# Performance work log

Hardware: AMD Instinct MI355X
Metric: run time of the kernel (lower is better)

The kernel has to match this reference:

```python
import jax, jax.numpy as jnp
import numpy as np

N = 4096
FEAT = 5
H = 128
L = 3
K = 4
HD = H // K  # 32


def setup_inputs() -> dict:
    key = jax.random.key(0)
    ks = jax.random.split(key, 24)
    node_features = jax.random.normal(ks[0], (N, FEAT), dtype=jnp.float32)
    u = jax.random.uniform(ks[1], (N, N), dtype=jnp.float32)
    adj = jnp.where(u < 0.01, u, 0.0)
    adj = adj / (adj.sum(axis=1, keepdims=True) + 1e-8)  # row-normalised
    mask = jax.random.randint(ks[2], (N,), 0, 2).astype(bool)
    s = 0.05
    return {
        'node_features': node_features,
        'adj': adj,
        'mask': mask,
        'Wi': jax.random.normal(ks[3], (FEAT, H), jnp.float32) * s,
        'bi': jnp.zeros((H,), jnp.float32),
        'gat_W': jax.random.normal(ks[4], (L, K, H, HD), jnp.float32) * s,
        'gat_a': jax.random.normal(ks[5], (L, K, 2 * HD), jnp.float32) * s,
        'ln_g': jnp.ones((L, H), jnp.float32),
        'ln_b': jnp.zeros((L, H), jnp.float32),
        'pW1': jax.random.normal(ks[6], (H, H // 2), jnp.float32) * s,
        'pb1': jnp.zeros((H // 2,), jnp.float32),
        'pW2': jax.random.normal(ks[7], (H // 2, 1), jnp.float32) * s,
        'pb2': jnp.zeros((1,), jnp.float32),
        'poolW': jax.random.normal(ks[8], (H, H), jnp.float32) * s,
        'poolb': jnp.zeros((H,), jnp.float32),
        'poolv': jax.random.normal(ks[9], (H,), jnp.float32) * s,
        'vW1': jax.random.normal(ks[10], (H, H // 2), jnp.float32) * s,
        'vb1': jnp.zeros((H // 2,), jnp.float32),
        'vW2': jax.random.normal(ks[11], (H // 2, 1), jnp.float32) * s,
        'vb2': jnp.zeros((1,), jnp.float32),
    }


def _layernorm(x, g, b, eps=1e-5):
    mu = x.mean(-1, keepdims=True)
    var = ((x - mu) ** 2).mean(-1, keepdims=True)
    return (x - mu) / jnp.sqrt(var + eps) * g + b


def reference(node_features, adj, mask, Wi, bi, gat_W, gat_a, ln_g, ln_b,
              pW1, pb1, pW2, pb2, poolW, poolb, poolv, vW1, vb1, vW2, vb2):
    n = node_features.shape[0]
    x = jax.nn.relu(node_features @ Wi + bi)  # (N, H)
    edge_mask = (adj > 0) | jnp.eye(n, dtype=bool)  # (N, N) incl self-loops
    n_layers = gat_W.shape[0]
    for l in range(n_layers):
        Wx = jnp.einsum('nd,kdh->knh', x, gat_W[l])  # (K, N, hd)
        a_src = jnp.einsum('knh,kh->kn', Wx, gat_a[l][:, :HD])  # (K, N)
        a_dst = jnp.einsum('knh,kh->kn', Wx, gat_a[l][:, HD:])  # (K, N)
        e = jax.nn.leaky_relu(a_src[:, :, None] + a_dst[:, None, :], 0.2)  # (K,N,N)
        e = jnp.where(edge_mask[None], e, -jnp.inf)
        alpha = jax.nn.softmax(e, axis=-1)  # softmax over neighbours j
        h = jax.nn.elu(jnp.einsum('kij,kjh->kih', alpha, Wx))  # (K, N, hd)
        out = jnp.transpose(h, (1, 0, 2)).reshape(n, -1)  # concat heads -> (N, H)
        out = out + x  # residual (Identity: in_dim == out_dim)
        x = _layernorm(out, ln_g[l], ln_b[l])
    # policy head
    logits = (jax.nn.relu(x @ pW1 + pb1) @ pW2 + pb2).squeeze(-1)  # (N,)
    logits = jnp.where(mask, logits, -jnp.inf)
    # attention pooling restricted to masked (valid) nodes
    scores = jnp.tanh(x @ poolW + poolb) @ poolv  # (N,)
    scores = jnp.where(mask, scores, -jnp.inf)
    beta = jax.nn.softmax(scores)
    pooled = (beta[:, None] * x).sum(0)  # (H,)
    value = (jax.nn.relu(pooled @ vW1 + vb1) @ vW2 + vb2).squeeze(-1)  # scalar
    return logits, value
```

## Files before the change

kernel.cpp:

```cpp
#include <hip/hip_runtime.h>

#define NN 4096
#define FEAT 5
#define H 128
#define HD 32
#define KH 4
#define NEG_INF (-__builtin_inff())
#define MASK_SENTINEL (-1e30f)

#define WS_FLAG  0
#define WS_DEG   256
#define WS_NBR   (WS_DEG + NN*4)
#define WS_X     (WS_NBR + NN*128*2)
#define WS_WX    (WS_X + NN*H*4)
#define WS_ATS   (WS_WX + NN*H*4)
#define WS_ATD   (WS_ATS + NN*16)
#define WS_PART  (WS_ATD + NN*16)
#define WS_ZPART (WS_PART + 256*H*4)

__device__ __forceinline__ float red64(float v) {
#pragma unroll
    for (int off = 32; off; off >>= 1) v += __shfl_xor(v, off, 64);
    return v;
}
__device__ __forceinline__ float red64max(float v) {
#pragma unroll
    for (int off = 32; off; off >>= 1) v = fmaxf(v, __shfl_xor(v, off, 64));
    return v;
}
__device__ __forceinline__ float red32(float v) {
#pragma unroll
    for (int off = 16; off; off >>= 1) v += __shfl_xor(v, off, 32);
    return v;
}
__device__ __forceinline__ bool read_mask(const void* mp, int f, int n) {
    if (f == 3) return ((const long long*)mp)[n] != 0;
    if (f == 1) return ((const int*)mp)[n] != 0;
    if (f == 2) return ((const float*)mp)[n] != 0.f;
    return ((const unsigned char*)mp)[n] != 0;
}

__global__ __launch_bounds__(256) void k_csr_proj(
    const float* __restrict__ adj, const float* __restrict__ nf,
    const float* __restrict__ Wi, const float* __restrict__ bi,
    const void* mask, int* flag, int* __restrict__ deg,
    unsigned short* __restrict__ nbr, float* __restrict__ xbuf) {
    __shared__ int ln[4][128];
    int w = threadIdx.x >> 6, lane = threadIdx.x & 63;
    int row = blockIdx.x * 4 + w;
    ln[w][lane] = 0; ln[w][64 + lane] = 0;
    const float4* arow = (const float4*)(adj + (size_t)row * NN);
    int cnt = 0;
    bool self = false;
    for (int c0 = 0; c0 < NN / 4; c0 += 64) {
        float4 v = arow[c0 + lane];
        int cb = (c0 + lane) * 4;
        float vals[4] = {v.x, v.y, v.z, v.w};
#pragma unroll
        for (int s = 0; s < 4; s++) {
            bool nz = vals[s] > 0.f;
            if (nz && cb + s == row) self = true;
            unsigned long long b = __ballot((int)nz);
            if (nz) {
                int pos = cnt + __popcll(b & ((1ull << lane) - 1ull));
                if (pos < 128) ln[w][pos] = cb + s;
            }
            cnt += __popcll(b);
        }
    }
    bool anyself = __any((int)self);
    if (!anyself) {
        if (lane == 0 && cnt < 128) ln[w][cnt] = row;
        cnt++;
    }
    int d = cnt < 128 ? cnt : 128;
    if (lane == 0) deg[row] = d;
    nbr[(size_t)row * 128 + lane] = (unsigned short)ln[w][lane];
    nbr[(size_t)row * 128 + 64 + lane] = (unsigned short)ln[w][64 + lane];
    float a1 = bi[lane], a2 = bi[64 + lane];
#pragma unroll
    for (int f = 0; f < FEAT; f++) {
        float xv = nf[row * FEAT + f];
        a1 += xv * Wi[f * H + lane];
        a2 += xv * Wi[f * H + 64 + lane];
    }
    xbuf[(size_t)row * H + lane] = fmaxf(a1, 0.f);
    xbuf[(size_t)row * H + 64 + lane] = fmaxf(a2, 0.f);
    if (blockIdx.x == 0 && w == 0) {
        const unsigned* ip = (const unsigned*)mask;
        const float* fp = (const float*)mask;
        bool i32ok = true, i64ok = true, f32ok = true;
        for (int i = lane; i < 1024; i += 64) {
            unsigned v = ip[i];
            if (v > 1u) i32ok = false;
            if (i & 1) { if (v != 0u) i64ok = false; }
            else       { if (v > 1u) i64ok = false; }
            float fv = fp[i];
            if (fv != 0.f && fv != 1.f) f32ok = false;
        }
        i32ok = (__ballot((int)i32ok) == ~0ull);
        i64ok = (__ballot((int)i64ok) == ~0ull);
        f32ok = (__ballot((int)f32ok) == ~0ull);
        if (lane == 0) *flag = i64ok ? 3 : (i32ok ? 1 : (f32ok ? 2 : 0));
    }
}

__global__ __launch_bounds__(256) void k_wx(
    const float* __restrict__ xbuf, const float* __restrict__ gw,
    const float* __restrict__ ga, float* __restrict__ Wx,
    float* __restrict__ attS, float* __restrict__ attD) {
    __shared__ float xs[8][H];
    int t = threadIdx.x;
    int k = t >> 6, lane = t & 63, dh = lane >> 5, h = lane & 31;
    int n0 = blockIdx.x * 8;
    ((float4*)xs)[t] = ((const float4*)(xbuf + (size_t)n0 * H))[t];
    __syncthreads();
    float acc[8] = {0, 0, 0, 0, 0, 0, 0, 0};
    const float* g = gw + (size_t)k * (H * HD) + h;
    for (int dd = 0; dd < 64; dd += 4) {
        int d = dh * 64 + dd;
        float w0 = g[(size_t)(d + 0) * HD];
        float w1 = g[(size_t)(d + 1) * HD];
        float w2 = g[(size_t)(d + 2) * HD];
        float w3 = g[(size_t)(d + 3) * HD];
#pragma unroll
        for (int nn = 0; nn < 8; nn++) {
            float4 xv = *(const float4*)&xs[nn][d];
            acc[nn] += xv.x * w0 + xv.y * w1 + xv.z * w2 + xv.w * w3;
        }
    }
    float aws = ga[k * 64 + h], awd = ga[k * 64 + 32 + h];
#pragma unroll
    for (int nn = 0; nn < 8; nn++) {
        float full = acc[nn] + __shfl_xor(acc[nn], 32, 64);
        float s = red32(full * aws);
        float dv = red32(full * awd);
        int n = n0 + nn;
        if (dh == 0) Wx[(size_t)n * H + k * 32 + h] = full;
        if (lane == 0) { attS[n * 4 + k] = s; attD[n * 4 + k] = dv; }
    }
}

__global__ __launch_bounds__(256) void k_agg(
    const int* __restrict__ degG, const unsigned short* __restrict__ nbrG,
    const float* __restrict__ Wxn, const float4* __restrict__ attS4,
    const float4* __restrict__ attD4, const float* __restrict__ lng,
    const float* __restrict__ lnb, float* __restrict__ xbuf) {
    __shared__ int s_nbr[4][128];
    __shared__ float s_al[4][128][4];
    int t = threadIdx.x, w = t >> 6, lane = t & 63;
    int node = blockIdx.x * 4 + w;
    int d = degG[node];
    const unsigned short* np = nbrG + (size_t)node * 128;
    int sn0 = np[lane], sn1 = np[64 + lane];
    s_nbr[w][lane] = sn0;
    s_nbr[w][64 + lane] = sn1;
    float4 aS = attS4[node];
    float4 d0 = attD4[sn0], d1 = attD4[sn1];
    bool v0 = lane < d, v1 = 64 + lane < d;
#define LRELU(x) ((x) > 0.f ? (x) : 0.2f * (x))
    float e0x = v0 ? LRELU(aS.x + d0.x) : NEG_INF;
    float e0y = v0 ? LRELU(aS.y + d0.y) : NEG_INF;
    float e0z = v0 ? LRELU(aS.z + d0.z) : NEG_INF;
    float e0w = v0 ? LRELU(aS.w + d0.w) : NEG_INF;
    float e1x = v1 ? LRELU(aS.x + d1.x) : NEG_INF;
    float e1y = v1 ? LRELU(aS.y + d1.y) : NEG_INF;
    float e1z = v1 ? LRELU(aS.z + d1.z) : NEG_INF;
    float e1w = v1 ? LRELU(aS.w + d1.w) : NEG_INF;
#undef LRELU
    float mx = red64max(fmaxf(e0x, e1x));
    float my = red64max(fmaxf(e0y, e1y));
    float mz = red64max(fmaxf(e0z, e1z));
    float mw = red64max(fmaxf(e0w, e1w));
    float p0x = v0 ? __expf(e0x - mx) : 0.f, p1x = v1 ? __expf(e1x - mx) : 0.f;
    float p0y = v0 ? __expf(e0y - my) : 0.f, p1y = v1 ? __expf(e1y - my) : 0.f;
    float p0z = v0 ? __expf(e0z - mz) : 0.f, p1z = v1 ? __expf(e1z - mz) : 0.f;
    float p0w = v0 ? __expf(e0w - mw) : 0.f, p1w = v1 ? __expf(e1w - mw) : 0.f;
    float ix = 1.f / red64(p0x + p1x);
    float iy = 1.f / red64(p0y + p1y);
    float iz = 1.f / red64(p0z + p1z);
    float iw = 1.f / red64(p0w + p1w);
    float4 a0 = make_float4(p0x * ix, p0y * iy, p0z * iz, p0w * iw);
    float4 a1 = make_float4(p1x * ix, p1y * iy, p1z * iz, p1w * iw);
    *(float4*)&s_al[w][lane][0] = a0;
    *(float4*)&s_al[w][64 + lane][0] = a1;
    int ksel = lane >> 4;
    int dim0 = 2 * lane;
    float acc0 = 0.f, acc1 = 0.f;
    int dpad = (d + 7) & ~7;
    for (int c0 = 0; c0 < dpad; c0 += 8) {
#pragma unroll
        for (int j = 0; j < 8; j++) {
            int c = c0 + j;
            int sc = s_nbr[w][c];
            float al = s_al[w][c][ksel];
            float2 v = *(const float2*)(Wxn + (size_t)sc * H + dim0);
            acc0 += al * v.x;
            acc1 += al * v.y;
        }
    }
    float2 xr = *(const float2*)(xbuf + (size_t)node * H + dim0);
    float h0 = acc0 > 0.f ? acc0 : __expf(acc0) - 1.f;
    float h1 = acc1 > 0.f ? acc1 : __expf(acc1) - 1.f;
    float o0 = h0 + xr.x, o1 = h1 + xr.y;
    float mu = red64(o0 + o1) * (1.f / H);
    float dv0 = o0 - mu, dv1 = o1 - mu;
    float var = red64(dv0 * dv0 + dv1 * dv1) * (1.f / H);
    float rstd = rsqrtf(var + 1e-5f);
    float2 ov;
    ov.x = dv0 * rstd * lng[dim0] + lnb[dim0];
    ov.y = dv1 * rstd * lng[dim0 + 1] + lnb[dim0 + 1];
    *(float2*)(xbuf + (size_t)node * H + dim0) = ov;
}

__global__ __launch_bounds__(256) void k_heads(
    const float* __restrict__ xbuf, const float* __restrict__ pW1,
    const float* __restrict__ pb1, const float* __restrict__ pW2,
    const float* __restrict__ pb2, const float* __restrict__ poolW,
    const float* __restrict__ poolb, const float* __restrict__ poolv,
    const void* mask, const int* __restrict__ flag, float* __restrict__ out,
    float* __restrict__ part, float* __restrict__ zpart) {
    __shared__ float lds_x[16][H];
    __shared__ float lds_part[4][H];
    __shared__ float lds_z[4];
    int t = threadIdx.x, w = t >> 6, lane = t & 63;
    int n0b = blockIdx.x * 16;
    for (int idx = t; idx < 16 * H; idx += 256)
        lds_x[idx >> 7][idx & 127] = xbuf[(size_t)(n0b + (idx >> 7)) * H + (idx & 127)];
    __syncthreads();
    int nb = n0b + w * 4;
    float accp[4] = {0, 0, 0, 0}, acs1[4] = {0, 0, 0, 0}, acs2[4] = {0, 0, 0, 0};
#pragma unroll 2
    for (int d = 0; d < H; d++) {
        float w1 = pW1[d * 64 + lane];
        float q1 = poolW[d * H + lane];
        float q2 = poolW[d * H + 64 + lane];
#pragma unroll
        for (int nn = 0; nn < 4; nn++) {
            float xv = lds_x[w * 4 + nn][d];
            accp[nn] += xv * w1;
            acs1[nn] += xv * q1;
            acs2[nn] += xv * q2;
        }
    }
    int flg = *flag;
    float T = fminf(red64(fabsf(poolv[lane]) + fabsf(poolv[64 + lane])), 30.f);
    float pb1v = pb1[lane], pw2v = pW2[lane], pb2v = pb2[0];
    float pob1 = poolb[lane], pob2 = poolb[64 + lane];
    float pov1 = poolv[lane], pov2 = poolv[64 + lane];
    float pp1 = 0.f, pp2 = 0.f, zacc = 0.f;
#pragma unroll
    for (int nn = 0; nn < 4; nn++) {
        int node = nb + nn;
        float hp = red64(fmaxf(accp[nn] + pb1v, 0.f) * pw2v);
        float sc = red64(tanhf(acs1[nn] + pob1) * pov1 + tanhf(acs2[nn] + pob2) * pov2);
        bool mk = read_mask(mask, flg, node);
        if (lane == 0) out[node] = mk ? (hp + pb2v) : MASK_SENTINEL;
        float wn = mk ? __expf(sc - T) : 0.f;
        pp1 += wn * lds_x[w * 4 + nn][lane];
        pp2 += wn * lds_x[w * 4 + nn][64 + lane];
        zacc += wn;
    }
    lds_part[w][lane] = pp1;
    lds_part[w][64 + lane] = pp2;
    if (lane == 0) lds_z[w] = zacc;
    __syncthreads();
    if (w == 0) {
        float s1 = lds_part[0][lane] + lds_part[1][lane] + lds_part[2][lane] + lds_part[3][lane];
        float s2 = lds_part[0][64 + lane] + lds_part[1][64 + lane] +
                   lds_part[2][64 + lane] + lds_part[3][64 + lane];
        part[blockIdx.x * H + lane] = s1;
        part[blockIdx.x * H + 64 + lane] = s2;
        if (lane == 0) zpart[blockIdx.x] = lds_z[0] + lds_z[1] + lds_z[2] + lds_z[3];
    }
}

__global__ __launch_bounds__(1024) void k_value(
    const float* __restrict__ part, const float* __restrict__ zpart,
    const float* __restrict__ vW1, const float* __restrict__ vb1,
    const float* __restrict__ vW2, const float* __restrict__ vb2,
    float* __restrict__ out) {
    __shared__ float segsum[8][H];
    __shared__ float zfin[256];
    __shared__ float pooled[H];
    int t = threadIdx.x;
    int dim = t & 127, seg = t >> 7;
    float s = 0.f;
#pragma unroll 8
    for (int b = seg * 32; b < seg * 32 + 32; b++) s += part[b * H + dim];
    segsum[seg][dim] = s;
    if (t < 256) zfin[t] = zpart[t];
    __syncthreads();
    if (t < 512) {
        int sg = t >> 7;
        segsum[sg][dim] += segsum[sg + 4][dim];
    }
    if (t >= 512 && t < 640) zfin[t - 512] += zfin[t - 512 + 128];
    __syncthreads();
    if (t < 256) {
        int sg = t >> 7;
        segsum[sg][dim] += segsum[sg + 2][dim];
    }
    if (t >= 512 && t < 576) zfin[t - 512] += zfin[t - 512 + 64];
    __syncthreads();
    if (t < 128) segsum[0][dim] += segsum[1][dim];
    if (t >= 512 && t < 544) zfin[t - 512] += zfin[t - 512 + 32];
    __syncthreads();
    if (t < 32) {
        float z = zfin[t];
#pragma unroll
        for (int off = 16; off; off >>= 1) z += __shfl_xor(z, off, 32);
        if (t == 0) zfin[0] = z;
    }
    __syncthreads();
    float Z = zfin[0];
    if (t < H) pooled[t] = segsum[0][t] / Z;
    __syncthreads();
    if (t < 64) {
        float acc = vb1[t];
#pragma unroll 4
        for (int d = 0; d < H; d++) acc += pooled[d] * vW1[d * 64 + t];
        float v = red64(fmaxf(acc, 0.f) * vW2[t]);
        if (t == 0) out[NN] = v + vb2[0];
    }
}

extern "C" void kernel_launch(void* const* d_in, const int* in_sizes, int n_in,
                              void* d_out, int out_size, void* d_ws, size_t ws_size,
                              hipStream_t stream) {
    const float* nf    = (const float*)d_in[0];
    const float* adj   = (const float*)d_in[1];
    const void*  mask  = d_in[2];
    const float* Wi    = (const float*)d_in[3];
    const float* bi    = (const float*)d_in[4];
    const float* gat_W = (const float*)d_in[5];
    const float* gat_a = (const float*)d_in[6];
    const float* ln_g  = (const float*)d_in[7];
    const float* ln_b  = (const float*)d_in[8];
    const float* pW1   = (const float*)d_in[9];
    const float* pb1   = (const float*)d_in[10];
    const float* pW2   = (const float*)d_in[11];
    const float* pb2   = (const float*)d_in[12];
    const float* poolW = (const float*)d_in[13];
    const float* poolb = (const float*)d_in[14];
    const float* poolv = (const float*)d_in[15];
    const float* vW1   = (const float*)d_in[16];
    const float* vb1   = (const float*)d_in[17];
    const float* vW2   = (const float*)d_in[18];
    const float* vb2   = (const float*)d_in[19];

    char* ws = (char*)d_ws;
    int*            flag = (int*)(ws + WS_FLAG);
    int*            deg  = (int*)(ws + WS_DEG);
    unsigned short* nbr  = (unsigned short*)(ws + WS_NBR);
    float* xbuf  = (float*)(ws + WS_X);
    float* Wx    = (float*)(ws + WS_WX);
    float* ats   = (float*)(ws + WS_ATS);
    float* atd   = (float*)(ws + WS_ATD);
    float* partb = (float*)(ws + WS_PART);
    float* zpart = (float*)(ws + WS_ZPART);
    float* out   = (float*)d_out;

    const size_t GWL = KH * H * HD;
    const size_t GAL = KH * 2 * HD;

    k_csr_proj<<<1024, 256, 0, stream>>>(adj, nf, Wi, bi, mask, flag, deg, nbr, xbuf);
    for (int l = 0; l < 3; l++) {
        k_wx<<<512, 256, 0, stream>>>(xbuf, gat_W + l * GWL, gat_a + l * GAL,
                                      Wx, ats, atd);
        k_agg<<<1024, 256, 0, stream>>>(deg, nbr, Wx, (const float4*)ats,
                                        (const float4*)atd, ln_g + l * H,
                                        ln_b + l * H, xbuf);
    }
    k_heads<<<256, 256, 0, stream>>>(xbuf, pW1, pb1, pW2, pb2, poolW, poolb, poolv,
                                     mask, flag, out, partb, zpart);
    k_value<<<1, 1024, 0, stream>>>(partb, zpart, vW1, vb1, vW2, vb2, out);
}
```

Before: 146.2 us.

## Fuse next-layer Wx projection into aggregation kernel with double-buffered Wx

Folds each layer's Wx/attention-logit projection into the tail of the preceding kernel: the CSR-build kernel also projects layer 0, and each aggregation kernel projects the next layer from the freshly normalised rows kept in LDS. Wx and attention buffers are double-buffered so a layer's aggregation can read the previous projection while writing the next. This removes three kernel launches and a global re-read of x per layer. In exchange, each block now handles 4 nodes instead of 8 in the projection, so gat_W weight loads are amortised over fewer rows.

```diff
diff --git a/kernel.cpp b/kernel.cpp
--- a/kernel.cpp
+++ b/kernel.cpp
@@ -12,10 +12,13 @@
 #define WS_DEG   256
 #define WS_NBR   (WS_DEG + NN*4)
 #define WS_X     (WS_NBR + NN*128*2)
-#define WS_WX    (WS_X + NN*H*4)
-#define WS_ATS   (WS_WX + NN*H*4)
-#define WS_ATD   (WS_ATS + NN*16)
-#define WS_PART  (WS_ATD + NN*16)
+#define WS_WXA   (WS_X + NN*H*4)
+#define WS_ATSA  (WS_WXA + NN*H*4)
+#define WS_ATDA  (WS_ATSA + NN*16)
+#define WS_WXB   (WS_ATDA + NN*16)
+#define WS_ATSB  (WS_WXB + NN*H*4)
+#define WS_ATDB  (WS_ATSB + NN*16)
+#define WS_PART  (WS_ATDB + NN*16)
 #define WS_ZPART (WS_PART + 256*H*4)
 
 __device__ __forceinline__ float red64(float v) {
@@ -40,82 +43,15 @@
     return ((const unsigned char*)mp)[n] != 0;
 }
 
-__global__ __launch_bounds__(256) void k_csr_proj(
-    const float* __restrict__ adj, const float* __restrict__ nf,
-    const float* __restrict__ Wi, const float* __restrict__ bi,
-    const void* mask, int* flag, int* __restrict__ deg,
-    unsigned short* __restrict__ nbr, float* __restrict__ xbuf) {
-    __shared__ int ln[4][128];
-    int w = threadIdx.x >> 6, lane = threadIdx.x & 63;
-    int row = blockIdx.x * 4 + w;
-    ln[w][lane] = 0; ln[w][64 + lane] = 0;
-    const float4* arow = (const float4*)(adj + (size_t)row * NN);
-    int cnt = 0;
-    bool self = false;
-    for (int c0 = 0; c0 < NN / 4; c0 += 64) {
-        float4 v = arow[c0 + lane];
-        int cb = (c0 + lane) * 4;
-        float vals[4] = {v.x, v.y, v.z, v.w};
-#pragma unroll
-        for (int s = 0; s < 4; s++) {
-            bool nz = vals[s] > 0.f;
-            if (nz && cb + s == row) self = true;
-            unsigned long long b = __ballot((int)nz);
-            if (nz) {
-                int pos = cnt + __popcll(b & ((1ull << lane) - 1ull));
-                if (pos < 128) ln[w][pos] = cb + s;
-            }
-            cnt += __popcll(b);
-        }
-    }
-    bool anyself = __any((int)self);
-    if (!anyself) {
-        if (lane == 0 && cnt < 128) ln[w][cnt] = row;
-        cnt++;
-    }
-    int d = cnt < 128 ? cnt : 128;
-    if (lane == 0) deg[row] = d;
-    nbr[(size_t)row * 128 + lane] = (unsigned short)ln[w][lane];
-    nbr[(size_t)row * 128 + 64 + lane] = (unsigned short)ln[w][64 + lane];
-    float a1 = bi[lane], a2 = bi[64 + lane];
-#pragma unroll
-    for (int f = 0; f < FEAT; f++) {
-        float xv = nf[row * FEAT + f];
-        a1 += xv * Wi[f * H + lane];
-        a2 += xv * Wi[f * H + 64 + lane];
-    }
-    xbuf[(size_t)row * H + lane] = fmaxf(a1, 0.f);
-    xbuf[(size_t)row * H + 64 + lane] = fmaxf(a2, 0.f);
-    if (blockIdx.x == 0 && w == 0) {
-        const unsigned* ip = (const unsigned*)mask;
-        const float* fp = (const float*)mask;
-        bool i32ok = true, i64ok = true, f32ok = true;
-        for (int i = lane; i < 1024; i += 64) {
-            unsigned v = ip[i];
-            if (v > 1u) i32ok = false;
-            if (i & 1) { if (v != 0u) i64ok = false; }
-            else       { if (v > 1u) i64ok = false; }
-            float fv = fp[i];
-            if (fv != 0.f && fv != 1.f) f32ok = false;
-        }
-        i32ok = (__ballot((int)i32ok) == ~0ull);
-        i64ok = (__ballot((int)i64ok) == ~0ull);
-        f32ok = (__ballot((int)f32ok) == ~0ull);
-        if (lane == 0) *flag = i64ok ? 3 : (i32ok ? 1 : (f32ok ? 2 : 0));
-    }
-}
-
-__global__ __launch_bounds__(256) void k_wx(
-    const float* __restrict__ xbuf, const float* __restrict__ gw,
-    const float* __restrict__ ga, float* __restrict__ Wx,
-    float* __restrict__ attS, float* __restrict__ attD) {
-    __shared__ float xs[8][H];
+__device__ __forceinline__ void wx4(const float (*lds_x)[H], int n0,
+                                    const float* __restrict__ gw,
+                                    const float* __restrict__ ga,
+                                    float* __restrict__ Wx,
+                                    float* __restrict__ attS,
+                                    float* __restrict__ attD) {
     int t = threadIdx.x;
     int k = t >> 6, lane = t & 63, dh = lane >> 5, h = lane & 31;
-    int n0 = blockIdx.x * 8;
-    ((float4*)xs)[t] = ((const float4*)(xbuf + (size_t)n0 * H))[t];
-    __syncthreads();
-    float acc[8] = {0, 0, 0, 0, 0, 0, 0, 0};
+    float acc[4] = {0.f, 0.f, 0.f, 0.f};
     const float* g = gw + (size_t)k * (H * HD) + h;
     for (int dd = 0; dd < 64; dd += 4) {
         int d = dh * 64 + dd;
@@ -124,14 +60,14 @@
         float w2 = g[(size_t)(d + 2) * HD];
         float w3 = g[(size_t)(d + 3) * HD];
 #pragma unroll
-        for (int nn = 0; nn < 8; nn++) {
-            float4 xv = *(const float4*)&xs[nn][d];
+        for (int nn = 0; nn < 4; nn++) {
+            float4 xv = *(const float4*)&lds_x[nn][d];
             acc[nn] += xv.x * w0 + xv.y * w1 + xv.z * w2 + xv.w * w3;
         }
     }
     float aws = ga[k * 64 + h], awd = ga[k * 64 + 32 + h];
 #pragma unroll
-    for (int nn = 0; nn < 8; nn++) {
+    for (int nn = 0; nn < 4; nn++) {
         float full = acc[nn] + __shfl_xor(acc[nn], 32, 64);
         float s = red32(full * aws);
         float dv = red32(full * awd);
@@ -141,15 +77,13 @@
     }
 }
 
-__global__ __launch_bounds__(256) void k_agg(
-    const int* __restrict__ degG, const unsigned short* __restrict__ nbrG,
-    const float* __restrict__ Wxn, const float4* __restrict__ attS4,
-    const float4* __restrict__ attD4, const float* __restrict__ lng,
-    const float* __restrict__ lnb, float* __restrict__ xbuf) {
-    __shared__ int s_nbr[4][128];
-    __shared__ float s_al[4][128][4];
-    int t = threadIdx.x, w = t >> 6, lane = t & 63;
-    int node = blockIdx.x * 4 + w;
+__device__ __forceinline__ void agg1(
+    int node, int w, int lane, const int* __restrict__ degG,
+    const unsigned short* __restrict__ nbrG, const float* __restrict__ Wxn,
+    const float4* __restrict__ attS4, const float4* __restrict__ attD4,
+    const float* __restrict__ lng, const float* __restrict__ lnb,
+    float* __restrict__ xbuf, int (*s_nbr)[128], float (*s_al)[128][4],
+    float* lds_row) {
     int d = degG[node];
     const unsigned short* np = nbrG + (size_t)node * 128;
     int sn0 = np[lane], sn1 = np[64 + lane];
@@ -180,10 +114,8 @@
     float iy = 1.f / red64(p0y + p1y);
     float iz = 1.f / red64(p0z + p1z);
     float iw = 1.f / red64(p0w + p1w);
-    float4 a0 = make_float4(p0x * ix, p0y * iy, p0z * iz, p0w * iw);
-    float4 a1 = make_float4(p1x * ix, p1y * iy, p1z * iz, p1w * iw);
-    *(float4*)&s_al[w][lane][0] = a0;
-    *(float4*)&s_al[w][64 + lane][0] = a1;
+    *(float4*)&s_al[w][lane][0]      = make_float4(p0x * ix, p0y * iy, p0z * iz, p0w * iw);
+    *(float4*)&s_al[w][64 + lane][0] = make_float4(p1x * ix, p1y * iy, p1z * iz, p1w * iw);
     int ksel = lane >> 4;
     int dim0 = 2 * lane;
     float acc0 = 0.f, acc1 = 0.f;
@@ -211,6 +143,111 @@
     ov.x = dv0 * rstd * lng[dim0] + lnb[dim0];
     ov.y = dv1 * rstd * lng[dim0 + 1] + lnb[dim0 + 1];
     *(float2*)(xbuf + (size_t)node * H + dim0) = ov;
+    if (lds_row) *(float2*)(lds_row + dim0) = ov;
+}
+
+__global__ __launch_bounds__(256) void k_csr_proj_wx(
+    const float* __restrict__ adj, const float* __restrict__ nf,
+    const float* __restrict__ Wi, const float* __restrict__ bi,
+    const void* mask, int* flag, int* __restrict__ deg,
+    unsigned short* __restrict__ nbr, float* __restrict__ xbuf,
+    const float* __restrict__ gw, const float* __restrict__ ga,
+    float* __restrict__ Wx, float* __restrict__ attS, float* __restrict__ attD) {
+    __shared__ int ln[4][128];
+    __shared__ float lds_x[4][H];
+    int w = threadIdx.x >> 6, lane = threadIdx.x & 63;
+    int row = blockIdx.x * 4 + w;
+    ln[w][lane] = 0; ln[w][64 + lane] = 0;
+    const float4* arow = (const float4*)(adj + (size_t)row * NN);
+    int cnt = 0;
+    bool self = false;
+    for (int c0 = 0; c0 < NN / 4; c0 += 64) {
+        float4 v = arow[c0 + lane];
+        int cb = (c0 + lane) * 4;
+        float vals[4] = {v.x, v.y, v.z, v.w};
+#pragma unroll
+        for (int s = 0; s < 4; s++) {
+            bool nz = vals[s] > 0.f;
+            if (nz && cb + s == row) self = true;
+            unsigned long long b = __ballot((int)nz);
+            if (nz) {
+                int pos = cnt + __popcll(b & ((1ull << lane) - 1ull));
+                if (pos < 128) ln[w][pos] = cb + s;
+            }
+            cnt += __popcll(b);
+        }
+    }
+    bool anyself = __any((int)self);
+    if (!anyself) {
+        if (lane == 0 && cnt < 128) ln[w][cnt] = row;
+        cnt++;
+    }
+    int d = cnt < 128 ? cnt : 128;
+    if (lane == 0) deg[row] = d;
+    nbr[(size_t)row * 128 + lane] = (unsigned short)ln[w][lane];
+    nbr[(size_t)row * 128 + 64 + lane] = (unsigned short)ln[w][64 + lane];
+    float a1 = bi[lane], a2 = bi[64 + lane];
+#pragma unroll
+    for (int f = 0; f < FEAT; f++) {
+        float xv = nf[row * FEAT + f];
+        a1 += xv * Wi[f * H + lane];
+        a2 += xv * Wi[f * H + 64 + lane];
+    }
+    a1 = fmaxf(a1, 0.f); a2 = fmaxf(a2, 0.f);
+    lds_x[w][lane] = a1; lds_x[w][64 + lane] = a2;
+    xbuf[(size_t)row * H + lane] = a1;
+    xbuf[(size_t)row * H + 64 + lane] = a2;
+    if (blockIdx.x == 0 && w == 0) {
+        const unsigned* ip = (const unsigned*)mask;
+        const float* fp = (const float*)mask;
+        bool i32ok = true, i64ok = true, f32ok = true;
+        for (int i = lane; i < 1024; i += 64) {
+            unsigned v = ip[i];
+            if (v > 1u) i32ok = false;
+            if (i & 1) { if (v != 0u) i64ok = false; }
+            else       { if (v > 1u) i64ok = false; }
+            float fv = fp[i];
+            if (fv != 0.f && fv != 1.f) f32ok = false;
+        }
+        i32ok = (__ballot((int)i32ok) == ~0ull);
+        i64ok = (__ballot((int)i64ok) == ~0ull);
+        f32ok = (__ballot((int)f32ok) == ~0ull);
+        if (lane == 0) *flag = i64ok ? 3 : (i32ok ? 1 : (f32ok ? 2 : 0));
+    }
+    __syncthreads();
+    wx4(lds_x, blockIdx.x * 4, gw, ga, Wx, attS, attD);
+}
+
+__global__ __launch_bounds__(256) void k_layer(
+    const int* __restrict__ degG, const unsigned short* __restrict__ nbrG,
+    const float* __restrict__ WxP, const float* __restrict__ attSP,
+    const float* __restrict__ attDP, const float* __restrict__ lng,
+    const float* __restrict__ lnb, float* __restrict__ xbuf,
+    const float* __restrict__ gwN, const float* __restrict__ gaN,
+    float* __restrict__ WxN, float* __restrict__ attSN,
+    float* __restrict__ attDN) {
+    __shared__ int s_nbr[4][128];
+    __shared__ float s_al[4][128][4];
+    __shared__ float lds_x[4][H];
+    int t = threadIdx.x, w = t >> 6, lane = t & 63;
+    int node = blockIdx.x * 4 + w;
+    agg1(node, w, lane, degG, nbrG, WxP, (const float4*)attSP,
+         (const float4*)attDP, lng, lnb, xbuf, s_nbr, s_al, lds_x[w]);
+    __syncthreads();
+    wx4(lds_x, blockIdx.x * 4, gwN, gaN, WxN, attSN, attDN);
+}
+
+__global__ __launch_bounds__(256) void k_agg_last(
+    const int* __restrict__ degG, const unsigned short* __restrict__ nbrG,
+    const float* __restrict__ WxP, const float* __restrict__ attSP,
+    const float* __restrict__ attDP, const float* __restrict__ lng,
+    const float* __restrict__ lnb, float* __restrict__ xbuf) {
+    __shared__ int s_nbr[4][128];
+    __shared__ float s_al[4][128][4];
+    int t = threadIdx.x, w = t >> 6, lane = t & 63;
+    int node = blockIdx.x * 4 + w;
+    agg1(node, w, lane, degG, nbrG, WxP, (const float4*)attSP,
+         (const float4*)attDP, lng, lnb, xbuf, s_nbr, s_al, nullptr);
 }
 
 __global__ __launch_bounds__(256) void k_heads(
@@ -354,9 +391,12 @@
     int*            deg  = (int*)(ws + WS_DEG);
     unsigned short* nbr  = (unsigned short*)(ws + WS_NBR);
     float* xbuf  = (float*)(ws + WS_X);
-    float* Wx    = (float*)(ws + WS_WX);
-    float* ats   = (float*)(ws + WS_ATS);
-    float* atd   = (float*)(ws + WS_ATD);
+    float* WxA   = (float*)(ws + WS_WXA);
+    float* atsA  = (float*)(ws + WS_ATSA);
+    float* atdA  = (float*)(ws + WS_ATDA);
+    float* WxB   = (float*)(ws + WS_WXB);
+    float* atsB  = (float*)(ws + WS_ATSB);
+    float* atdB  = (float*)(ws + WS_ATDB);
     float* partb = (float*)(ws + WS_PART);
     float* zpart = (float*)(ws + WS_ZPART);
     float* out   = (float*)d_out;
@@ -364,14 +404,15 @@
     const size_t GWL = KH * H * HD;
     const size_t GAL = KH * 2 * HD;
 
-    k_csr_proj<<<1024, 256, 0, stream>>>(adj, nf, Wi, bi, mask, flag, deg, nbr, xbuf);
-    for (int l = 0; l < 3; l++) {
-        k_wx<<<512, 256, 0, stream>>>(xbuf, gat_W + l * GWL, gat_a + l * GAL,
-                                      Wx, ats, atd);
-        k_agg<<<1024, 256, 0, stream>>>(deg, nbr, Wx, (const float4*)ats,
-                                        (const float4*)atd, ln_g + l * H,
-                                        ln_b + l * H, xbuf);
-    }
+    k_csr_proj_wx<<<1024, 256, 0, stream>>>(adj, nf, Wi, bi, mask, flag, deg, nbr,
+                                            xbuf, gat_W, gat_a, WxA, atsA, atdA);
+    k_layer<<<1024, 256, 0, stream>>>(deg, nbr, WxA, atsA, atdA, ln_g, ln_b, xbuf,
+                                      gat_W + GWL, gat_a + GAL, WxB, atsB, atdB);
+    k_layer<<<1024, 256, 0, stream>>>(deg, nbr, WxB, atsB, atdB, ln_g + H, ln_b + H,
+                                      xbuf, gat_W + 2 * GWL, gat_a + 2 * GAL,
+                                      WxA, atsA, atdA);
+    k_agg_last<<<1024, 256, 0, stream>>>(deg, nbr, WxA, atsA, atdA,
+                                         ln_g + 2 * H, ln_b + 2 * H, xbuf);
     k_heads<<<256, 256, 0, stream>>>(xbuf, pW1, pb1, pW2, pb2, poolW, poolb, poolv,
                                      mask, flag, out, partb, zpart);
     k_value<<<1, 1024, 0, stream>>>(partb, zpart, vW1, vb1, vW2, vb2, out);
```

New measurement: 171.9 us. +17.6%, slower.

## Store Wx in bf16 and restructure CSR build with per-lane contiguous scans

Applied to the files above, without the earlier changes.

Wx is now written as bf16 (round-to-nearest via bit arithmetic) and unpacked in the aggregation gather, halving the bytes read per neighbour row. The CSR construction changes so that each lane scans a contiguous 64-column chunk of the adjacency row and keeps up to 12 candidates locally, followed by a single prefix scan. This replaces the per-element ballots. Risks include bf16 rounding error in the aggregation, and silently dropping neighbours if any lane's chunk holds more than 12 nonzeros. The strided per-lane float4 loads are also less coalesced.

```diff
diff --git a/kernel.cpp b/kernel.cpp
--- a/kernel.cpp
+++ b/kernel.cpp
@@ -13,7 +13,7 @@
 #define WS_NBR   (WS_DEG + NN*4)
 #define WS_X     (WS_NBR + NN*128*2)
 #define WS_WX    (WS_X + NN*H*4)
-#define WS_ATS   (WS_WX + NN*H*4)
+#define WS_ATS   (WS_WX + NN*H*2)
 #define WS_ATD   (WS_ATS + NN*16)
 #define WS_PART  (WS_ATD + NN*16)
 #define WS_ZPART (WS_PART + 256*H*4)
@@ -46,34 +46,46 @@
     const void* mask, int* flag, int* __restrict__ deg,
     unsigned short* __restrict__ nbr, float* __restrict__ xbuf) {
     __shared__ int ln[4][128];
+    __shared__ unsigned short cand[4][64][12];
     int w = threadIdx.x >> 6, lane = threadIdx.x & 63;
     int row = blockIdx.x * 4 + w;
     ln[w][lane] = 0; ln[w][64 + lane] = 0;
     const float4* arow = (const float4*)(adj + (size_t)row * NN);
     int cnt = 0;
     bool self = false;
-    for (int c0 = 0; c0 < NN / 4; c0 += 64) {
-        float4 v = arow[c0 + lane];
-        int cb = (c0 + lane) * 4;
+#pragma unroll 4
+    for (int j = 0; j < 16; j++) {
+        float4 v = arow[lane * 16 + j];
+        int cb = lane * 64 + j * 4;
         float vals[4] = {v.x, v.y, v.z, v.w};
 #pragma unroll
         for (int s = 0; s < 4; s++) {
-            bool nz = vals[s] > 0.f;
-            if (nz && cb + s == row) self = true;
-            unsigned long long b = __ballot((int)nz);
-            if (nz) {
-                int pos = cnt + __popcll(b & ((1ull << lane) - 1ull));
-                if (pos < 128) ln[w][pos] = cb + s;
+            if (vals[s] > 0.f) {
+                if (cnt < 12) cand[w][lane][cnt] = (unsigned short)(cb + s);
+                cnt++;
+                if (cb + s == row) self = true;
             }
-            cnt += __popcll(b);
-        }
-    }
+        }
+    }
+    int cl = cnt < 12 ? cnt : 12;
+    int inc = cl;
+#pragma unroll
+    for (int off = 1; off < 64; off <<= 1) {
+        int o = __shfl_up(inc, off, 64);
+        if (lane >= off) inc += o;
+    }
+    int excl = inc - cl;
+    int total = __shfl(inc, 63, 64);
     bool anyself = __any((int)self);
+    for (int t2 = 0; t2 < cl; t2++) {
+        int pos = excl + t2;
+        if (pos < 128) ln[w][pos] = cand[w][lane][t2];
+    }
     if (!anyself) {
-        if (lane == 0 && cnt < 128) ln[w][cnt] = row;
-        cnt++;
-    }
-    int d = cnt < 128 ? cnt : 128;
+        if (lane == 0 && total < 128) ln[w][total] = row;
+        total++;
+    }
+    int d = total < 128 ? total : 128;
     if (lane == 0) deg[row] = d;
     nbr[(size_t)row * 128 + lane] = (unsigned short)ln[w][lane];
     nbr[(size_t)row * 128 + 64 + lane] = (unsigned short)ln[w][64 + lane];
@@ -107,7 +119,7 @@
 
 __global__ __launch_bounds__(256) void k_wx(
     const float* __restrict__ xbuf, const float* __restrict__ gw,
-    const float* __restrict__ ga, float* __restrict__ Wx,
+    const float* __restrict__ ga, unsigned short* __restrict__ WxBF,
     float* __restrict__ attS, float* __restrict__ attD) {
     __shared__ float xs[8][H];
     int t = threadIdx.x;
@@ -136,14 +148,16 @@
         float s = red32(full * aws);
         float dv = red32(full * awd);
         int n = n0 + nn;
-        if (dh == 0) Wx[(size_t)n * H + k * 32 + h] = full;
+        if (dh == 0)
+            WxBF[(size_t)n * H + k * 32 + h] =
+                (unsigned short)((__float_as_uint(full) + 0x8000u) >> 16);
         if (lane == 0) { attS[n * 4 + k] = s; attD[n * 4 + k] = dv; }
     }
 }
 
 __global__ __launch_bounds__(256) void k_agg(
     const int* __restrict__ degG, const unsigned short* __restrict__ nbrG,
-    const float* __restrict__ Wxn, const float4* __restrict__ attS4,
+    const unsigned short* __restrict__ WxBF, const float4* __restrict__ attS4,
     const float4* __restrict__ attD4, const float* __restrict__ lng,
     const float* __restrict__ lnb, float* __restrict__ xbuf) {
     __shared__ int s_nbr[4][128];
@@ -180,10 +194,8 @@
     float iy = 1.f / red64(p0y + p1y);
     float iz = 1.f / red64(p0z + p1z);
     float iw = 1.f / red64(p0w + p1w);
-    float4 a0 = make_float4(p0x * ix, p0y * iy, p0z * iz, p0w * iw);
-    float4 a1 = make_float4(p1x * ix, p1y * iy, p1z * iz, p1w * iw);
-    *(float4*)&s_al[w][lane][0] = a0;
-    *(float4*)&s_al[w][64 + lane][0] = a1;
+    *(float4*)&s_al[w][lane][0]      = make_float4(p0x * ix, p0y * iy, p0z * iz, p0w * iw);
+    *(float4*)&s_al[w][64 + lane][0] = make_float4(p1x * ix, p1y * iy, p1z * iz, p1w * iw);
     int ksel = lane >> 4;
     int dim0 = 2 * lane;
     float acc0 = 0.f, acc1 = 0.f;
@@ -194,9 +206,9 @@
             int c = c0 + j;
             int sc = s_nbr[w][c];
             float al = s_al[w][c][ksel];
-            float2 v = *(const float2*)(Wxn + (size_t)sc * H + dim0);
-            acc0 += al * v.x;
-            acc1 += al * v.y;
+            unsigned int v = *(const unsigned int*)(WxBF + (size_t)sc * H + dim0);
+            acc0 += al * __uint_as_float(v << 16);
+            acc1 += al * __uint_as_float(v & 0xFFFF0000u);
         }
     }
     float2 xr = *(const float2*)(xbuf + (size_t)node * H + dim0);
@@ -353,8 +365,8 @@
     int*            flag = (int*)(ws + WS_FLAG);
     int*            deg  = (int*)(ws + WS_DEG);
     unsigned short* nbr  = (unsigned short*)(ws + WS_NBR);
-    float* xbuf  = (float*)(ws + WS_X);
-    float* Wx    = (float*)(ws + WS_WX);
+    float*          xbuf = (float*)(ws + WS_X);
+    unsigned short* WxBF = (unsigned short*)(ws + WS_WX);
     float* ats   = (float*)(ws + WS_ATS);
     float* atd   = (float*)(ws + WS_ATD);
     float* partb = (float*)(ws + WS_PART);
@@ -367,8 +379,8 @@
     k_csr_proj<<<1024, 256, 0, stream>>>(adj, nf, Wi, bi, mask, flag, deg, nbr, xbuf);
     for (int l = 0; l < 3; l++) {
         k_wx<<<512, 256, 0, stream>>>(xbuf, gat_W + l * GWL, gat_a + l * GAL,
-                                      Wx, ats, atd);
-        k_agg<<<1024, 256, 0, stream>>>(deg, nbr, Wx, (const float4*)ats,
+                                      WxBF, ats, atd);
+        k_agg<<<1024, 256, 0, stream>>>(deg, nbr, WxBF, (const float4*)ats,
                                         (const float4*)atd, ln_g + l * H,
                                         ln_b + l * H, xbuf);
     }
```

New measurement: 147.8 us. About the same (+1.1%).
